# Optimization experiments

Hardware: AMD Instinct MI355X
Metric: run time of the kernel (lower is better)

The kernel has to match this reference:

```python
import jax, jax.numpy as jnp
import numpy as np
from jax import lax

N, T, U, V = 32, 512, 100, 4096
BLANK = 0


def setup_inputs() -> dict:
    key = jax.random.key(0)
    k1, k2, k3, k4, k5 = jax.random.split(key, 5)
    encoder_out = jax.random.normal(k1, (N, T, V), dtype=jnp.float32)
    decoder_out = jax.random.normal(k2, (N, U + 1, V), dtype=jnp.float32)
    targets = jax.random.randint(k3, (N, U), 1, V)            # labels, never blank
    input_lengths = jax.random.randint(k4, (N,), T // 2, T + 1)
    target_lengths = jax.random.randint(k5, (N,), U // 2, U + 1)
    return {
        "encoder_out": encoder_out,
        "decoder_out": decoder_out,
        "targets": targets,
        "input_lengths": input_lengths,
        "target_lengths": target_lengths,
    }


def _logprob_single(enc, dec, y, in_len, tgt_len):
    # enc: (T, V)  dec: (U+1, V)  y: (U,)
    Um = y.shape[0]
    u_idx = jnp.arange(Um)
    # emit[t, u] = enc[t, y[u]] + dec[u, y[u]]  (cost of emitting label u+1 at time t)
    emit = enc[:, y] + dec[u_idx, y][None, :]          # (T, U)
    blank_e = enc[:, BLANK]                            # (T,)
    blank_d = dec[:, BLANK]                            # (U+1,)

    # t = 0 row: alpha[0, u] = sum_{k<u} emit[0, k]
    alpha0 = jnp.concatenate([jnp.zeros((1,), enc.dtype), jnp.cumsum(emit[0])])

    def row_step(alpha_prev, xs):
        be_prev, emit_t = xs
        # blank transition from row t-1 (same u)
        top = alpha_prev + be_prev + blank_d           # (U+1,)

        # label transition within row: alpha[u] = logaddexp(top[u], alpha[u-1] + emit_t[u-1])
        def u_step(carry, x):
            top_u, em = x
            a = jnp.logaddexp(top_u, carry + em)
            return a, a

        _, rest = lax.scan(u_step, top[0], (top[1:], emit_t))
        alpha = jnp.concatenate([top[:1], rest])
        return alpha, alpha

    _, rows = lax.scan(row_step, alpha0, (blank_e[:-1], emit[1:]))
    alphas = jnp.concatenate([alpha0[None, :], rows], axis=0)   # (T, U+1)

    # log p(y|x) = alpha[T-1, U] + enc[T-1, blank] + dec[U, blank] with true lengths
    return alphas[in_len - 1, tgt_len] + enc[in_len - 1, BLANK] + dec[tgt_len, BLANK]


def reference(encoder_out, decoder_out, targets, input_lengths, target_lengths):
    # reduction='none': returns per-utterance log p(y|x), shape (N,)
    return jax.vmap(_logprob_single)(encoder_out, decoder_out, targets,
                                     input_lengths, target_lengths)
```

## Files before the change

kernel.cpp:

```cpp
#include <hip/hip_runtime.h>

#define NB 32
#define TT 512
#define UU 100
#define UM 101
#define VV 4096
#define NEG (-1e30f)
#define PD 24
#define DMAX 672
#define L2E 1.4426950408889634f
#define LN2 0.6931471805599453f

__device__ __forceinline__ float vexp2(float x){ float r; asm("v_exp_f32 %0, %1" : "=v"(r) : "v"(x)); return r; }
__device__ __forceinline__ float vlog2(float x){ float r; asm("v_log_f32 %0, %1" : "=v"(r) : "v"(x)); return r; }

__device__ __forceinline__ float lae2(float a, float b) {
    float m  = fmaxf(a, b);
    float nd = fminf(a, b) - m;
    return m + vlog2(1.0f + vexp2(nd));
}

__global__ void prep_k(const float* __restrict__ enc, const float* __restrict__ dec,
                       const int* __restrict__ tgt,
                       float* __restrict__ blk, float* __restrict__ bdv,
                       float* __restrict__ dvx) {
    int n = blockIdx.x, tid = threadIdx.x;
    blk[n * TT + tid] = enc[((size_t)n * TT + tid) * VV] * L2E;
    if (tid < 128)
        bdv[n * 128 + tid] = (tid < UM) ? dec[((size_t)n * UM + tid) * VV] * L2E : 0.0f;
    if (tid < UU) {
        int y = tgt[n * UU + tid];
        dvx[n * UU + tid] = dec[((size_t)n * UM + tid) * VV + y] * L2E;
    }
}

__global__ void build_k(const float* __restrict__ enc, const int* __restrict__ tgt,
                        const int* __restrict__ ilen, const int* __restrict__ tlen,
                        const float* __restrict__ dvx, float2* __restrict__ st) {
    int n = blockIdx.y;
    int d = blockIdx.x * 4 + (threadIdx.x >> 6);
    int lane = threadIdx.x & 63;
    int tin = ilen[n], tg = tlen[n];
    const float* encn = enc + (size_t)n * TT * VV;
    float e0 = NEG, e1 = NEG;
    {
        int u = 2 * lane, t = d - u;
        if (u >= 1 && u <= tg && t >= 0 && t < tin)
            e0 = fmaf(encn[(size_t)t * VV + tgt[n * UU + u - 1]], L2E, dvx[n * UU + u - 1]);
    }
    {
        int u = 2 * lane + 1, t = d - u;
        if (u <= tg && t >= 0 && t < tin)
            e1 = fmaf(encn[(size_t)t * VV + tgt[n * UU + u - 1]], L2E, dvx[n * UU + u - 1]);
    }
    st[((size_t)n * DMAX + d) * 64 + lane] = make_float2(e0, e1);
}

__global__ __launch_bounds__(64, 1) void dp_k(const int* __restrict__ ilen,
                                              const int* __restrict__ tlen,
                                              const float2* __restrict__ st,
                                              const float* __restrict__ blk,
                                              const float* __restrict__ bdv,
                                              float* __restrict__ out) {
    int n = blockIdx.x;
    int lane = threadIdx.x;
    int tin = ilen[n], tg = tlen[n];
    int dend = tin - 1 + tg;

    __shared__ float blkL[864];
    for (int i = lane; i < 864; i += 64) blkL[i] = NEG;
    __syncthreads();
    for (int t = lane; t < TT; t += 64) blkL[128 + t] = blk[n * TT + t];
    __syncthreads();

    float bd0 = bdv[n * 128 + 2 * lane];
    float bd1 = bdv[n * 128 + 2 * lane + 1];
    const float2* sp = st + ((size_t)n * DMAX) * 64 + lane;
    int ib = 126 - 2 * lane;
    bool cap0 = (2 * lane == tg), cap1 = (2 * lane + 1 == tg);
    bool fx16 = (lane == 16), fx32 = (lane == 32), fx48 = (lane == 48);

    float a0 = (lane == 0) ? 0.0f : NEG;
    float a1 = NEG;
    float res = NEG;

    float Ae0[PD], Ae1[PD], Ab0[PD], Ab1[PD];
    float Be0[PD], Be1[PD], Bb0[PD], Bb1[PD];

#define LOADR(E0, E1, B0, B1, K, DD)                                   \
    {                                                                   \
        int dc = min((DD), DMAX - 1);                                   \
        float2 ev = sp[(size_t)dc * 64];                                \
        float b1s = blkL[ib + dc];                                      \
        float b0s = blkL[ib + dc + 1];                                  \
        E0[K] = ev.x; E1[K] = ev.y;                                     \
        B0[K] = b0s + bd0; B1[K] = b1s + bd1;                           \
    }

    auto STEP = [&](float e0, float e1, float bb0, float bb1, int dd) {
        int sh = __builtin_amdgcn_update_dpp(__float_as_int(NEG), __float_as_int(a1),
                                             0x111, 0xF, 0xF, false);
        float s15 = __int_as_float(__builtin_amdgcn_readlane(__float_as_int(a1), 15));
        float s31 = __int_as_float(__builtin_amdgcn_readlane(__float_as_int(a1), 31));
        float s47 = __int_as_float(__builtin_amdgcn_readlane(__float_as_int(a1), 47));
        float l0 = __int_as_float(sh);
        l0 = fx16 ? s15 : l0;
        l0 = fx32 ? s31 : l0;
        l0 = fx48 ? s47 : l0;
        float bt0 = a0 + bb0, et0 = l0 + e0;
        float bt1 = a1 + bb1, et1 = a0 + e1;
        a0 = lae2(bt0, et0);
        a1 = lae2(bt1, et1);
        if (dd == dend) { if (cap0) res = a0; if (cap1) res = a1; }
    };

#pragma unroll
    for (int k = 0; k < PD; ++k) LOADR(Ae0, Ae1, Ab0, Ab1, k, 1 + k);
    __builtin_amdgcn_sched_barrier(0);

    for (int d = 1; d <= dend; d += 2 * PD) {
#pragma unroll
        for (int k = 0; k < PD; ++k) LOADR(Be0, Be1, Bb0, Bb1, k, d + PD + k);
        __builtin_amdgcn_sched_barrier(0);
#pragma unroll
        for (int k = 0; k < PD; ++k) STEP(Ae0[k], Ae1[k], Ab0[k], Ab1[k], d + k);
        __builtin_amdgcn_sched_barrier(0);
#pragma unroll
        for (int k = 0; k < PD; ++k) LOADR(Ae0, Ae1, Ab0, Ab1, k, d + 2 * PD + k);
        __builtin_amdgcn_sched_barrier(0);
#pragma unroll
        for (int k = 0; k < PD; ++k) STEP(Be0[k], Be1[k], Bb0[k], Bb1[k], d + PD + k);
        __builtin_amdgcn_sched_barrier(0);
    }

    float fin  = blkL[128 + tin - 1];
    float bdtg = bdv[n * 128 + tg];
    if (cap0 | cap1) out[n] = (res + fin + bdtg) * LN2;
#undef LOADR
}

extern "C" void kernel_launch(void* const* d_in, const int* in_sizes, int n_in,
                              void* d_out, int out_size, void* d_ws, size_t ws_size,
                              hipStream_t hs) {
    const float* enc  = (const float*)d_in[0];
    const float* dec  = (const float*)d_in[1];
    const int*   tgt  = (const int*)d_in[2];
    const int*   ilen = (const int*)d_in[3];
    const int*   tlen = (const int*)d_in[4];
    float* out = (float*)d_out;

    float2* st  = (float2*)d_ws;
    float*  blk = (float*)(st + (size_t)NB * DMAX * 64);
    float*  bdv = blk + NB * TT;
    float*  dvx = bdv + NB * 128;

    hipLaunchKernelGGL(prep_k,  dim3(NB), dim3(512), 0, hs, enc, dec, tgt, blk, bdv, dvx);
    hipLaunchKernelGGL(build_k, dim3(DMAX / 4, NB), dim3(256), 0, hs,
                       enc, tgt, ilen, tlen, dvx, st);
    hipLaunchKernelGGL(dp_k,    dim3(NB), dim3(64), 0, hs, ilen, tlen, st, blk, bdv, out);
}
```

Before: 87.45 us.

## Fuse prep, emission build and DP into one producer-consumer kernel

Replaces three launches (prep, emission staging to global workspace, wavefront DP) with one kernel per utterance. Fifteen producer waves gather emission values into a double-buffered LDS window of 64 diagonals while wave 0 runs the anti-diagonal DP on the previous window. This removes the global round-trip and two launch overheads. In exchange there is a block-wide barrier every window, and the DP wave now depends on producers keeping pace with the gathers.

Measured after the change: 71.90 us. 1.22x faster.

```diff
diff --git a/kernel.cpp b/kernel.cpp
--- a/kernel.cpp
+++ b/kernel.cpp
@@ -6,8 +6,7 @@
 #define UM 101
 #define VV 4096
 #define NEG (-1e30f)
-#define PD 24
-#define DMAX 672
+#define WIN 64
 #define L2E 1.4426950408889634f
 #define LN2 0.6931471805599453f
 
@@ -20,123 +19,129 @@
     return m + vlog2(1.0f + vexp2(nd));
 }
 
-__global__ void prep_k(const float* __restrict__ enc, const float* __restrict__ dec,
-                       const int* __restrict__ tgt,
-                       float* __restrict__ blk, float* __restrict__ bdv,
-                       float* __restrict__ dvx) {
-    int n = blockIdx.x, tid = threadIdx.x;
-    blk[n * TT + tid] = enc[((size_t)n * TT + tid) * VV] * L2E;
-    if (tid < 128)
-        bdv[n * 128 + tid] = (tid < UM) ? dec[((size_t)n * UM + tid) * VV] * L2E : 0.0f;
+__global__ __launch_bounds__(1024, 1) void fused_k(
+        const float* __restrict__ enc, const float* __restrict__ dec,
+        const int* __restrict__ tgt, const int* __restrict__ ilen,
+        const int* __restrict__ tlen, float* __restrict__ out) {
+    __shared__ float em[2][WIN][128];
+    __shared__ float blkL[864];
+    __shared__ int   tgtL[UU];
+    __shared__ float dvxL[UU];
+
+    int n = blockIdx.x;
+    int tid = threadIdx.x;
+    int tin = ilen[n], tg = tlen[n];
+    int dend = tin - 1 + tg;
+    int E = (dend + WIN - 1) / WIN;
+    const float* encn = enc + (size_t)n * TT * VV;
+
+    for (int i = tid; i < 864; i += 1024)
+        blkL[i] = (i >= 128 && i < 128 + TT) ? encn[(size_t)(i - 128) * VV] * L2E : NEG;
     if (tid < UU) {
         int y = tgt[n * UU + tid];
-        dvx[n * UU + tid] = dec[((size_t)n * UM + tid) * VV + y] * L2E;
+        tgtL[tid] = y;
+        dvxL[tid] = dec[((size_t)n * UM + tid) * VV + y] * L2E;
     }
-}
-
-__global__ void build_k(const float* __restrict__ enc, const int* __restrict__ tgt,
-                        const int* __restrict__ ilen, const int* __restrict__ tlen,
-                        const float* __restrict__ dvx, float2* __restrict__ st) {
-    int n = blockIdx.y;
-    int d = blockIdx.x * 4 + (threadIdx.x >> 6);
-    int lane = threadIdx.x & 63;
-    int tin = ilen[n], tg = tlen[n];
-    const float* encn = enc + (size_t)n * TT * VV;
-    float e0 = NEG, e1 = NEG;
-    {
-        int u = 2 * lane, t = d - u;
-        if (u >= 1 && u <= tg && t >= 0 && t < tin)
-            e0 = fmaf(encn[(size_t)t * VV + tgt[n * UU + u - 1]], L2E, dvx[n * UU + u - 1]);
-    }
-    {
-        int u = 2 * lane + 1, t = d - u;
-        if (u <= tg && t >= 0 && t < tin)
-            e1 = fmaf(encn[(size_t)t * VV + tgt[n * UU + u - 1]], L2E, dvx[n * UU + u - 1]);
-    }
-    st[((size_t)n * DMAX + d) * 64 + lane] = make_float2(e0, e1);
-}
-
-__global__ __launch_bounds__(64, 1) void dp_k(const int* __restrict__ ilen,
-                                              const int* __restrict__ tlen,
-                                              const float2* __restrict__ st,
-                                              const float* __restrict__ blk,
-                                              const float* __restrict__ bdv,
-                                              float* __restrict__ out) {
-    int n = blockIdx.x;
-    int lane = threadIdx.x;
-    int tin = ilen[n], tg = tlen[n];
-    int dend = tin - 1 + tg;
-
-    __shared__ float blkL[864];
-    for (int i = lane; i < 864; i += 64) blkL[i] = NEG;
-    __syncthreads();
-    for (int t = lane; t < TT; t += 64) blkL[128 + t] = blk[n * TT + t];
     __syncthreads();
 
-    float bd0 = bdv[n * 128 + 2 * lane];
-    float bd1 = bdv[n * 128 + 2 * lane + 1];
-    const float2* sp = st + ((size_t)n * DMAX) * 64 + lane;
-    int ib = 126 - 2 * lane;
+    int wave = tid >> 6;
+    int lane = tid & 63;
+
+    auto FILLWIN = [&](int w, int baseDp) {
+        int pid = tid - 64;
+        float* emw = &em[w][0][0];
+#pragma unroll
+        for (int it = 0; it < 9; ++it) {
+            int idx = pid + it * 960;
+            if (idx < WIN * 128) {
+                int dm = idx >> 7, u = idx & 127;
+                int d = baseDp + dm + 1;
+                int t = d - u;
+                float val = NEG;
+                if (u >= 1 && u <= tg && t >= 0 && t < tin)
+                    val = fmaf(encn[(size_t)t * VV + tgtL[u - 1]], L2E, dvxL[u - 1]);
+                emw[idx] = val;
+            }
+        }
+    };
+
+    if (wave != 0) FILLWIN(0, 0);
+
+    int u0c = min(2 * lane, UM - 1), u1c = min(2 * lane + 1, UM - 1);
+    float bd0 = dec[((size_t)n * UM + u0c) * VV] * L2E;
+    float bd1 = dec[((size_t)n * UM + u1c) * VV] * L2E;
+    int ib0 = 127 - 2 * lane;
     bool cap0 = (2 * lane == tg), cap1 = (2 * lane + 1 == tg);
     bool fx16 = (lane == 16), fx32 = (lane == 32), fx48 = (lane == 48);
-
     float a0 = (lane == 0) ? 0.0f : NEG;
     float a1 = NEG;
     float res = NEG;
 
-    float Ae0[PD], Ae1[PD], Ab0[PD], Ab1[PD];
-    float Be0[PD], Be1[PD], Bb0[PD], Bb1[PD];
+    float Ae0[8], Ae1[8], Ab0[8], Ab1[8], Be0[8], Be1[8], Bb0[8], Bb1[8];
 
-#define LOADR(E0, E1, B0, B1, K, DD)                                   \
-    {                                                                   \
-        int dc = min((DD), DMAX - 1);                                   \
-        float2 ev = sp[(size_t)dc * 64];                                \
-        float b1s = blkL[ib + dc];                                      \
-        float b0s = blkL[ib + dc + 1];                                  \
-        E0[K] = ev.x; E1[K] = ev.y;                                     \
-        B0[K] = b0s + bd0; B1[K] = b1s + bd1;                           \
+    auto REFILL = [&](float (&Re0)[8], float (&Re1)[8], float (&Rb0)[8], float (&Rb1)[8],
+                      int j0, int dbase, const float* emb) {
+#pragma unroll
+        for (int k = 0; k < 8; ++k) {
+            int dm = j0 + k;
+            float2 ev = *(const float2*)(emb + dm * 128 + 2 * lane);
+            int d = dbase + dm + 1;
+            Re0[k] = ev.x; Re1[k] = ev.y;
+            Rb0[k] = blkL[ib0 + d] + bd0;
+            Rb1[k] = blkL[ib0 + d - 1] + bd1;
+        }
+        __builtin_amdgcn_sched_barrier(0);
+    };
+
+    auto STEPS = [&](float (&Re0)[8], float (&Re1)[8], float (&Rb0)[8], float (&Rb1)[8],
+                     int j0, int dbase) {
+#pragma unroll
+        for (int k = 0; k < 8; ++k) {
+            int dd = dbase + j0 + k + 1;
+            int sh = __builtin_amdgcn_update_dpp(__float_as_int(NEG), __float_as_int(a1),
+                                                 0x111, 0xF, 0xF, false);
+            float s15 = __int_as_float(__builtin_amdgcn_readlane(__float_as_int(a1), 15));
+            float s31 = __int_as_float(__builtin_amdgcn_readlane(__float_as_int(a1), 31));
+            float s47 = __int_as_float(__builtin_amdgcn_readlane(__float_as_int(a1), 47));
+            float l0 = __int_as_float(sh);
+            l0 = fx16 ? s15 : l0;
+            l0 = fx32 ? s31 : l0;
+            l0 = fx48 ? s47 : l0;
+            float bt0 = a0 + Rb0[k], et0 = l0 + Re0[k];
+            float bt1 = a1 + Rb1[k], et1 = a0 + Re1[k];
+            a0 = lae2(bt0, et0);
+            a1 = lae2(bt1, et1);
+            if (dd == dend) { if (cap0) res = a0; if (cap1) res = a1; }
+        }
+        __builtin_amdgcn_sched_barrier(0);
+    };
+
+    __syncthreads();
+
+    for (int e = 0; e < E; ++e) {
+        if (wave == 0) {
+            int dbase = e * WIN;
+            const float* emb = &em[e & 1][0][0];
+            REFILL(Ae0, Ae1, Ab0, Ab1, 0, dbase, emb);
+            REFILL(Be0, Be1, Bb0, Bb1, 8, dbase, emb);  STEPS(Ae0, Ae1, Ab0, Ab1, 0, dbase);
+            REFILL(Ae0, Ae1, Ab0, Ab1, 16, dbase, emb); STEPS(Be0, Be1, Bb0, Bb1, 8, dbase);
+            REFILL(Be0, Be1, Bb0, Bb1, 24, dbase, emb); STEPS(Ae0, Ae1, Ab0, Ab1, 16, dbase);
+            REFILL(Ae0, Ae1, Ab0, Ab1, 32, dbase, emb); STEPS(Be0, Be1, Bb0, Bb1, 24, dbase);
+            REFILL(Be0, Be1, Bb0, Bb1, 40, dbase, emb); STEPS(Ae0, Ae1, Ab0, Ab1, 32, dbase);
+            REFILL(Ae0, Ae1, Ab0, Ab1, 48, dbase, emb); STEPS(Be0, Be1, Bb0, Bb1, 40, dbase);
+            REFILL(Be0, Be1, Bb0, Bb1, 56, dbase, emb); STEPS(Ae0, Ae1, Ab0, Ab1, 48, dbase);
+            STEPS(Be0, Be1, Bb0, Bb1, 56, dbase);
+        } else {
+            FILLWIN((e + 1) & 1, (e + 1) * WIN);
+        }
+        __syncthreads();
     }
 
-    auto STEP = [&](float e0, float e1, float bb0, float bb1, int dd) {
-        int sh = __builtin_amdgcn_update_dpp(__float_as_int(NEG), __float_as_int(a1),
-                                             0x111, 0xF, 0xF, false);
-        float s15 = __int_as_float(__builtin_amdgcn_readlane(__float_as_int(a1), 15));
-        float s31 = __int_as_float(__builtin_amdgcn_readlane(__float_as_int(a1), 31));
-        float s47 = __int_as_float(__builtin_amdgcn_readlane(__float_as_int(a1), 47));
-        float l0 = __int_as_float(sh);
-        l0 = fx16 ? s15 : l0;
-        l0 = fx32 ? s31 : l0;
-        l0 = fx48 ? s47 : l0;
-        float bt0 = a0 + bb0, et0 = l0 + e0;
-        float bt1 = a1 + bb1, et1 = a0 + e1;
-        a0 = lae2(bt0, et0);
-        a1 = lae2(bt1, et1);
-        if (dd == dend) { if (cap0) res = a0; if (cap1) res = a1; }
-    };
-
-#pragma unroll
-    for (int k = 0; k < PD; ++k) LOADR(Ae0, Ae1, Ab0, Ab1, k, 1 + k);
-    __builtin_amdgcn_sched_barrier(0);
-
-    for (int d = 1; d <= dend; d += 2 * PD) {
-#pragma unroll
-        for (int k = 0; k < PD; ++k) LOADR(Be0, Be1, Bb0, Bb1, k, d + PD + k);
-        __builtin_amdgcn_sched_barrier(0);
-#pragma unroll
-        for (int k = 0; k < PD; ++k) STEP(Ae0[k], Ae1[k], Ab0[k], Ab1[k], d + k);
-        __builtin_amdgcn_sched_barrier(0);
-#pragma unroll
-        for (int k = 0; k < PD; ++k) LOADR(Ae0, Ae1, Ab0, Ab1, k, d + 2 * PD + k);
-        __builtin_amdgcn_sched_barrier(0);
-#pragma unroll
-        for (int k = 0; k < PD; ++k) STEP(Be0[k], Be1[k], Bb0[k], Bb1[k], d + PD + k);
-        __builtin_amdgcn_sched_barrier(0);
+    if (wave == 0 && (cap0 | cap1)) {
+        float fin  = blkL[128 + tin - 1];
+        float bdtg = dec[((size_t)n * UM + tg) * VV] * L2E;
+        out[n] = (res + fin + bdtg) * LN2;
     }
-
-    float fin  = blkL[128 + tin - 1];
-    float bdtg = bdv[n * 128 + tg];
-    if (cap0 | cap1) out[n] = (res + fin + bdtg) * LN2;
-#undef LOADR
 }
 
 extern "C" void kernel_launch(void* const* d_in, const int* in_sizes, int n_in,
@@ -149,13 +154,6 @@
     const int*   tlen = (const int*)d_in[4];
     float* out = (float*)d_out;
 
-    float2* st  = (float2*)d_ws;
-    float*  blk = (float*)(st + (size_t)NB * DMAX * 64);
-    float*  bdv = blk + NB * TT;
-    float*  dvx = bdv + NB * 128;
-
-    hipLaunchKernelGGL(prep_k,  dim3(NB), dim3(512), 0, hs, enc, dec, tgt, blk, bdv, dvx);
-    hipLaunchKernelGGL(build_k, dim3(DMAX / 4, NB), dim3(256), 0, hs,
-                       enc, tgt, ilen, tlen, dvx, st);
-    hipLaunchKernelGGL(dp_k,    dim3(NB), dim3(64), 0, hs, ilen, tlen, st, blk, bdv, out);
+    hipLaunchKernelGGL(fused_k, dim3(NB), dim3(1024), 0, hs,
+                       enc, dec, tgt, ilen, tlen, out);
 }
```
